# Performance work log

Hardware: AMD Instinct MI355X
Metric: run time of the kernel (lower is better)

Reference implementation:

```python
import jax, jax.numpy as jnp
import numpy as np

B, L, D, H, I = 4, 2048, 768, 12, 3072
HD = D // H  # 64
EPS = 1e-5


def _ln(x, g, b):
    mu = jnp.mean(x, axis=-1, keepdims=True)
    var = jnp.var(x, axis=-1, keepdims=True)
    return (x - mu) * jax.lax.rsqrt(var + EPS) * g + b


def setup_inputs() -> dict:
    key = jax.random.key(0)
    ks = jax.random.split(key, 8)
    s = 0.02
    return {
        "x": jax.random.normal(ks[0], (B, L, D), dtype=jnp.float32),
        "attention_mask": jnp.ones((B, L), dtype=bool),
        "ln1_g": jnp.ones((D,), jnp.float32),
        "ln1_b": jnp.zeros((D,), jnp.float32),
        "w_qkv": jax.random.normal(ks[1], (D, 3 * D), jnp.float32) * s,
        "b_qkv": jnp.zeros((3 * D,), jnp.float32),
        "w_o": jax.random.normal(ks[2], (D, D), jnp.float32) * s,
        "b_o": jnp.zeros((D,), jnp.float32),
        "ln2_g": jnp.ones((D,), jnp.float32),
        "ln2_b": jnp.zeros((D,), jnp.float32),
        "w1": jax.random.normal(ks[3], (D, I), jnp.float32) * s,
        "b1": jnp.zeros((I,), jnp.float32),
        "w2": jax.random.normal(ks[4], (I, D), jnp.float32) * s,
        "b2": jnp.zeros((D,), jnp.float32),
    }


def reference(x, attention_mask, ln1_g, ln1_b, w_qkv, b_qkv, w_o, b_o,
              ln2_g, ln2_b, w1, b1, w2, b2):
    # pre-LN + fused qkv projection
    h = _ln(x, ln1_g, ln1_b)
    qkv = h @ w_qkv + b_qkv                      # [B,L,3D]
    qkv = qkv.reshape(B, L, H, 3 * HD)           # chunk per-head: first HD=q, then k, then v
    q, k, v = qkv[..., :HD], qkv[..., HD:2 * HD], qkv[..., 2 * HD:]
    # NOTE: original divides by head_dim (q.size(-1)), NOT sqrt(head_dim)
    scores = jnp.einsum('blhd,bmhd->bhlm', q, k) / HD   # [B,H,L,L]
    causal = jnp.tril(jnp.ones((L, L), dtype=bool))
    full_mask = attention_mask[:, None, None, :] & causal
    scores = jnp.where(full_mask, scores, -jnp.inf)
    p = jax.nn.softmax(scores, axis=-1)
    attn = jnp.einsum('bhlm,bmhd->blhd', p, v).reshape(B, L, D)
    out_attn = attn @ w_o + b_o + x
    # FFN: Sequential(Linear, Linear, GELU, Dropout) -> GELU applied LAST (faithful to source)
    h2 = _ln(out_attn, ln2_g, ln2_b)
    ff = jax.nn.gelu((h2 @ w1 + b1) @ w2 + b2, approximate=False)
    return out_attn + ff
```

## Files before the change

### kernel.cpp

```cpp
#include <hip/hip_runtime.h>
#include <stdint.h>

typedef __attribute__((ext_vector_type(8))) short short8;
typedef __attribute__((ext_vector_type(4))) float f32x4;

typedef const void __attribute__((address_space(1)))* gas1_t;
typedef void __attribute__((address_space(3)))* las3_t;
#define GLL16(g, l) __builtin_amdgcn_global_load_lds((gas1_t)(const void*)(g), (las3_t)(void*)(l), 16, 0, 0)

__device__ __forceinline__ unsigned short f2bf(float x){
  union { float f; unsigned u; } c; c.f = x;
  return (unsigned short)((c.u + 0x7fffu + ((c.u >> 16) & 1u)) >> 16);
}

__device__ __forceinline__ short8 pack_bf16x8(f32x4 a, f32x4 b){
  union { unsigned u[4]; short8 s8; } r;
  asm("v_cvt_pk_bf16_f32 %0, %1, %2" : "=v"(r.u[0]) : "v"(a[0]), "v"(a[1]));
  asm("v_cvt_pk_bf16_f32 %0, %1, %2" : "=v"(r.u[1]) : "v"(a[2]), "v"(a[3]));
  asm("v_cvt_pk_bf16_f32 %0, %1, %2" : "=v"(r.u[2]) : "v"(b[0]), "v"(b[1]));
  asm("v_cvt_pk_bf16_f32 %0, %1, %2" : "=v"(r.u[3]) : "v"(b[2]), "v"(b[3]));
  return r.s8;
}

constexpr int Bc = 4, Lc = 2048, Dc = 768, Hc = 12, HDc = 64, Ic = 3072;
constexpr int Mrows = Bc * Lc;
constexpr int N3 = 3 * Dc;

__global__ void transpose_w(const float* __restrict__ W, unsigned short* __restrict__ Wt, int K, int N){
  __shared__ float t[32][33];
  int n0 = blockIdx.x * 32, k0 = blockIdx.y * 32;
  int tx = threadIdx.x, ty = threadIdx.y;
  #pragma unroll
  for (int j = 0; j < 4; ++j)
    t[ty + 8*j][tx] = W[(size_t)(k0 + ty + 8*j) * N + n0 + tx];
  __syncthreads();
  #pragma unroll
  for (int j = 0; j < 4; ++j)
    Wt[(size_t)(n0 + ty + 8*j) * K + k0 + tx] = f2bf(t[tx][ty + 8*j]);
}

__global__ void transpose_v(const unsigned short* __restrict__ qkv, unsigned short* __restrict__ vt){
  __shared__ unsigned short t[32][33];
  int l0 = blockIdx.x * 32, d0 = blockIdx.y * 32;
  int bh = blockIdx.z; int b = bh / Hc, h = bh - b * Hc;
  int tx = threadIdx.x, ty = threadIdx.y;
  const unsigned short* src = qkv + (size_t)b * Lc * N3 + h * 192 + 128;
  #pragma unroll
  for (int j = 0; j < 4; ++j)
    t[ty + 8*j][tx] = src[(size_t)(l0 + ty + 8*j) * N3 + d0 + tx];
  __syncthreads();
  unsigned short* dst = vt + (size_t)bh * 64 * Lc;
  #pragma unroll
  for (int j = 0; j < 4; ++j)
    dst[(size_t)(d0 + ty + 8*j) * Lc + l0 + tx] = t[tx][ty + 8*j];
}

__global__ __launch_bounds__(256) void ln_kernel(const float* __restrict__ x, const float* __restrict__ g,
                                                 const float* __restrict__ bta, unsigned short* __restrict__ out){
  int row = blockIdx.x, tid = threadIdx.x;
  const float* xr = x + (size_t)row * 768;
  float v0 = xr[tid], v1 = xr[tid + 256], v2 = xr[tid + 512];
  float s = v0 + v1 + v2;
  float ss = v0*v0 + v1*v1 + v2*v2;
  #pragma unroll
  for (int o = 32; o > 0; o >>= 1){ s += __shfl_xor(s, o); ss += __shfl_xor(ss, o); }
  __shared__ float red[8];
  int w = tid >> 6;
  if ((tid & 63) == 0){ red[w] = s; red[4 + w] = ss; }
  __syncthreads();
  s  = red[0] + red[1] + red[2] + red[3];
  ss = red[4] + red[5] + red[6] + red[7];
  float mu  = s * (1.f / 768.f);
  float var = ss * (1.f / 768.f) - mu * mu;
  float rs  = rsqrtf(var + 1e-5f);
  unsigned short* orow = out + (size_t)row * 768;
  orow[tid]       = f2bf((v0 - mu) * rs * g[tid]       + bta[tid]);
  orow[tid + 256] = f2bf((v1 - mu) * rs * g[tid + 256] + bta[tid + 256]);
  orow[tid + 512] = f2bf((v2 - mu) * rs * g[tid + 512] + bta[tid + 512]);
}

template<int MODE>
__global__ __launch_bounds__(256, 2) void gemm_bt(
    const unsigned short* __restrict__ A, const unsigned short* __restrict__ Bt,
    const float* __restrict__ bias, const float* __restrict__ res,
    void* __restrict__ outp, int Kdim, int Ndim)
{
  __shared__ __align__(16) unsigned short Als[2][128 * 64];
  __shared__ __align__(16) unsigned short Bls[2][128 * 64];
  int tid = threadIdx.x, w = tid >> 6, lane = tid & 63;
  int g = lane >> 4, r16 = lane & 15;

  int nwg = gridDim.x * gridDim.y;
  int flat = blockIdx.y * gridDim.x + blockIdx.x;
  int cpx = nwg >> 3;
  int swz = (flat & 7) * cpx + (flat >> 3);
  int bx = swz % gridDim.x, by = swz / gridDim.x;
  int m0 = by * 128, n0 = bx * 128;
  int wr = (w >> 1) * 64, wc = (w & 1) * 64;

  f32x4 acc[4][4];
  #pragma unroll
  for (int m = 0; m < 4; ++m)
    #pragma unroll
    for (int n = 0; n < 4; ++n) acc[m][n] = f32x4{0.f, 0.f, 0.f, 0.f};

  int lrow = lane >> 3;
  int gsw8 = ((lane & 7) ^ lrow) * 8;
  auto stage = [&](int buf, int kt){
    int k0 = kt * 64;
    #pragma unroll
    for (int i = 0; i < 4; ++i){
      int c = w * 4 + i;
      int row = c * 8 + lrow;
      GLL16(A  + (size_t)(m0 + row) * Kdim + k0 + gsw8, &Als[buf][c * 512]);
      GLL16(Bt + (size_t)(n0 + row) * Kdim + k0 + gsw8, &Bls[buf][c * 512]);
    }
  };

  int nk = Kdim >> 6;
  stage(0, 0);
  int cur = 0;
  for (int kt = 0; kt < nk; ++kt){
    __builtin_amdgcn_s_barrier();
    if (kt + 1 < nk){
      stage(cur ^ 1, kt + 1);
      asm volatile("s_waitcnt vmcnt(8)" ::: "memory");
    } else {
      asm volatile("s_waitcnt vmcnt(0)" ::: "memory");
    }
    __builtin_amdgcn_s_barrier();

    #pragma unroll
    for (int ks = 0; ks < 2; ++ks){
      short8 af[4], bfv[4];
      #pragma unroll
      for (int m = 0; m < 4; ++m){
        int r = wr + m*16 + r16;
        af[m] = *(const short8*)&Als[cur][r * 64 + (((ks*4 + g) ^ (r & 7)) << 3)];
      }
      #pragma unroll
      for (int n = 0; n < 4; ++n){
        int r = wc + n*16 + r16;
        bfv[n] = *(const short8*)&Bls[cur][r * 64 + (((ks*4 + g) ^ (r & 7)) << 3)];
      }
      #pragma unroll
      for (int m = 0; m < 4; ++m)
        #pragma unroll
        for (int n = 0; n < 4; ++n)
          acc[m][n] = __builtin_amdgcn_mfma_f32_16x16x32_bf16(af[m], bfv[n], acc[m][n], 0, 0, 0);
    }
    cur ^= 1;
  }

  #pragma unroll
  for (int n = 0; n < 4; ++n){
    int col = n0 + wc + n*16 + r16;
    float bv = bias[col];
    #pragma unroll
    for (int m = 0; m < 4; ++m){
      #pragma unroll
      for (int j = 0; j < 4; ++j){
        int rowg = m0 + wr + m*16 + g*4 + j;
        size_t idx = (size_t)rowg * Ndim + col;
        float v = acc[m][n][j] + bv;
        if (MODE == 0){
          ((unsigned short*)outp)[idx] = f2bf(v);
        } else if (MODE == 1){
          ((float*)outp)[idx] = v + res[idx];
        } else {
          float ge = 0.5f * v * (1.0f + erff(v * 0.70710678118f));
          ((float*)outp)[idx] = res[idx] + ge;
        }
      }
    }
  }
}

__global__ __launch_bounds__(256, 2) void attn_kernel(const unsigned short* __restrict__ qkv,
                                                      const unsigned short* __restrict__ vt,
                                                      unsigned short* __restrict__ attn_out){
  int qt = 31 - blockIdx.y;
  int bh = blockIdx.x;
  int b = bh / Hc, h = bh - b * Hc;
  int tid = threadIdx.x, w = tid >> 6, lane = tid & 63;
  int g = lane >> 4, r16 = lane & 15;
  const unsigned short* base  = qkv + (size_t)b * Lc * N3 + h * 192;
  const unsigned short* vbase = vt + (size_t)bh * 64 * Lc;

  __shared__ __align__(16) unsigned short Kls[2][64 * 64];
  __shared__ __align__(16) unsigned short Vls[2][64 * 64];
  __shared__ __align__(16) float Pls[4][16 * 64];

  int qw = qt * 64 + w * 16;
  short8 qf[2];
  #pragma unroll
  for (int dh = 0; dh < 2; ++dh)
    qf[dh] = *(const short8*)(base + (size_t)(qw + r16) * N3 + dh*32 + g*8);

  f32x4 o[4];
  #pragma unroll
  for (int nd = 0; nd < 4; ++nd) o[nd] = f32x4{0.f, 0.f, 0.f, 0.f};
  float l_part[4] = {0.f, 0.f, 0.f, 0.f};

  float* Pw = &Pls[w][0];
  constexpr float SM_SCALE = 0.022542110013890052f;

  int lrow = lane >> 3, csw8 = ((lane & 7) ^ lrow) * 8;
  auto stage = [&](int buf, int kt){
    #pragma unroll
    for (int i = 0; i < 2; ++i){
      int r0 = (w * 2 + i) * 8;
      int row = r0 + lrow;
      GLL16(base  + (size_t)(kt*64 + row) * N3 + 64 + csw8, &Kls[buf][r0 * 64]);
      GLL16(vbase + (size_t)row * Lc + kt*64 + csw8,        &Vls[buf][r0 * 64]);
    }
  };

  auto compute_tile = [&](int cur, int kt, bool diag){
    f32x4 s[4];
    #pragma unroll
    for (int nk = 0; nk < 4; ++nk) s[nk] = f32x4{0.f,0.f,0.f,0.f};
    #pragma unroll
    for (int nk = 0; nk < 4; ++nk){
      int krow = nk*16 + r16;
      #pragma unroll
      for (int dh = 0; dh < 2; ++dh){
        short8 kf = *(const short8*)&Kls[cur][krow * 64 + (((dh*4 + g) ^ (krow & 7)) << 3)];
        s[nk] = __builtin_amdgcn_mfma_f32_16x16x32_bf16(qf[dh], kf, s[nk], 0, 0, 0);
      }
    }
    int qv = qw + g*4;
    #pragma unroll
    for (int nk = 0; nk < 4; ++nk){
      int kc = kt*64 + nk*16 + r16;
      #pragma unroll
      for (int j = 0; j < 4; ++j){
        float t = s[nk][j] * SM_SCALE;
        if (diag) t = (kc <= qv + j) ? t : -1e30f;
        float p = __builtin_amdgcn_exp2f(t);
        l_part[j] += p;
        int row = g*4 + j, col = nk*16 + r16;
        Pw[(row << 6) + ((((col >> 2) ^ (row & 7)) << 2) | (col & 3))] = p;
      }
    }
    asm volatile("" ::: "memory");
    #pragma unroll
    for (int ks = 0; ks < 2; ++ks){
      int gr0 = (ks*8 + g*2) ^ (r16 & 7);
      int gr1 = (ks*8 + g*2 + 1) ^ (r16 & 7);
      f32x4 pa = *(const f32x4*)&Pw[(r16 << 6) + (gr0 << 2)];
      f32x4 pb = *(const f32x4*)&Pw[(r16 << 6) + (gr1 << 2)];
      short8 pf = pack_bf16x8(pa, pb);
      #pragma unroll
      for (int nd = 0; nd < 4; ++nd){
        int vrow = nd*16 + r16;
        short8 vf = *(const short8*)&Vls[cur][vrow * 64 + (((ks*4 + g) ^ (vrow & 7)) << 3)];
        o[nd] = __builtin_amdgcn_mfma_f32_16x16x32_bf16(pf, vf, o[nd], 0, 0, 0);
      }
    }
  };

  stage(0, 0);
  __syncthreads();
  int cur = 0;
  for (int kt = 0; kt < qt; ++kt){
    stage(cur ^ 1, kt + 1);
    compute_tile(cur, kt, false);
    __syncthreads();
    cur ^= 1;
  }
  compute_tile(cur, qt, true);

  #pragma unroll
  for (int off = 8; off > 0; off >>= 1)
    #pragma unroll
    for (int j = 0; j < 4; ++j) l_part[j] += __shfl_xor(l_part[j], off);
  float inv[4];
  #pragma unroll
  for (int j = 0; j < 4; ++j) inv[j] = 1.0f / l_part[j];

  unsigned short* ob = attn_out + (size_t)b * Lc * Dc + h * HDc;
  #pragma unroll
  for (int nd = 0; nd < 4; ++nd)
    #pragma unroll
    for (int j = 0; j < 4; ++j){
      int q2 = qw + g*4 + j;
      ob[(size_t)q2 * Dc + nd*16 + r16] = f2bf(o[nd][j] * inv[j]);
    }
}

extern "C" void kernel_launch(void* const* d_in, const int* in_sizes, int n_in,
                              void* d_out, int out_size, void* d_ws, size_t ws_size,
                              hipStream_t stream){
  const float* x     = (const float*)d_in[0];
  const float* ln1_g = (const float*)d_in[2];
  const float* ln1_b = (const float*)d_in[3];
  const float* w_qkv = (const float*)d_in[4];
  const float* b_qkv = (const float*)d_in[5];
  const float* w_o   = (const float*)d_in[6];
  const float* b_o   = (const float*)d_in[7];
  const float* ln2_g = (const float*)d_in[8];
  const float* ln2_b = (const float*)d_in[9];
  const float* w1    = (const float*)d_in[10];
  const float* b1    = (const float*)d_in[11];
  const float* w2    = (const float*)d_in[12];
  const float* b2    = (const float*)d_in[13];

  char* ws = (char*)d_ws;
  size_t off = 0;
  auto alloc = [&](size_t bytes){ void* p = ws + off; off += (bytes + 255) & ~(size_t)255; return p; };
  unsigned short* wqkv_t = (unsigned short*)alloc((size_t)N3 * Dc * 2);
  unsigned short* wo_t   = (unsigned short*)alloc((size_t)Dc * Dc * 2);
  unsigned short* w1_t   = (unsigned short*)alloc((size_t)Ic * Dc * 2);
  unsigned short* w2_t   = (unsigned short*)alloc((size_t)Dc * Ic * 2);
  unsigned short* hbuf   = (unsigned short*)alloc((size_t)Mrows * Dc * 2);
  float*          oattn  = (float*)alloc((size_t)Mrows * Dc * 4);
  unsigned short* vtb    = (unsigned short*)alloc((size_t)Bc * Hc * HDc * Lc * 2);
  char*           big    = (char*)alloc((size_t)Mrows * Ic * 2);
  unsigned short* qkv    = (unsigned short*)big;
  unsigned short* attn_o = (unsigned short*)(big + (size_t)Mrows * N3 * 2);
  unsigned short* ff1    = (unsigned short*)big;

  dim3 tb(32, 8, 1);
  transpose_w<<<dim3(N3/32, Dc/32), tb, 0, stream>>>(w_qkv, wqkv_t, Dc, N3);
  transpose_w<<<dim3(Dc/32, Dc/32), tb, 0, stream>>>(w_o,   wo_t,   Dc, Dc);
  transpose_w<<<dim3(Ic/32, Dc/32), tb, 0, stream>>>(w1,    w1_t,   Dc, Ic);
  transpose_w<<<dim3(Dc/32, Ic/32), tb, 0, stream>>>(w2,    w2_t,   Ic, Dc);

  ln_kernel<<<dim3(Mrows), dim3(256), 0, stream>>>(x, ln1_g, ln1_b, hbuf);

  gemm_bt<0><<<dim3(N3/128, Mrows/128), dim3(256), 0, stream>>>(hbuf, wqkv_t, b_qkv, nullptr, (void*)qkv, Dc, N3);

  transpose_v<<<dim3(Lc/32, HDc/32, Bc*Hc), tb, 0, stream>>>(qkv, vtb);

  attn_kernel<<<dim3(Bc*Hc, Lc/64), dim3(256), 0, stream>>>(qkv, vtb, attn_o);

  gemm_bt<1><<<dim3(Dc/128, Mrows/128), dim3(256), 0, stream>>>(attn_o, wo_t, b_o, x, (void*)oattn, Dc, Dc);

  ln_kernel<<<dim3(Mrows), dim3(256), 0, stream>>>(oattn, ln2_g, ln2_b, hbuf);

  gemm_bt<0><<<dim3(Ic/128, Mrows/128), dim3(256), 0, stream>>>(hbuf, w1_t, b1, nullptr, (void*)ff1, Dc, Ic);

  gemm_bt<2><<<dim3(Dc/128, Mrows/128), dim3(256), 0, stream>>>(ff1, w2_t, b2, oattn, d_out, Ic, Dc);
}
```

Before: 280.8 us.

## Replace 128x128 GEMM with 256x256 eight-wave kernel and interleaved LDS/MFMA phases

All four GEMMs move from a 128x128 tile with 4 waves to a 256x256 tile with 8 waves, each wave computing 128x64. The inner k-loop is split into four phases that alternate LDS fragment loads with MFMA bursts, separated by barriers and s_setprio, so that fragment reads overlap with matrix math and register pressure stays bounded. The larger tiles cut global and LDS traffic per FLOP. In exchange, LDS use reaches 128KB per block and the N=768 GEMMs launch only 96 workgroups, which may leave many CUs idle.

```diff
diff --git a/kernel.cpp b/kernel.cpp
--- a/kernel.cpp
+++ b/kernel.cpp
@@ -80,27 +80,27 @@
 }
 
 template<int MODE>
-__global__ __launch_bounds__(256, 2) void gemm_bt(
+__global__ __launch_bounds__(512, 2) void gemm256(
     const unsigned short* __restrict__ A, const unsigned short* __restrict__ Bt,
     const float* __restrict__ bias, const float* __restrict__ res,
     void* __restrict__ outp, int Kdim, int Ndim)
 {
-  __shared__ __align__(16) unsigned short Als[2][128 * 64];
-  __shared__ __align__(16) unsigned short Bls[2][128 * 64];
+  __shared__ __align__(16) unsigned short Als[2][256 * 64];
+  __shared__ __align__(16) unsigned short Bls[2][256 * 64];
   int tid = threadIdx.x, w = tid >> 6, lane = tid & 63;
   int g = lane >> 4, r16 = lane & 15;
+  int wm = w >> 2, wn = w & 3;
 
   int nwg = gridDim.x * gridDim.y;
   int flat = blockIdx.y * gridDim.x + blockIdx.x;
   int cpx = nwg >> 3;
   int swz = (flat & 7) * cpx + (flat >> 3);
   int bx = swz % gridDim.x, by = swz / gridDim.x;
-  int m0 = by * 128, n0 = bx * 128;
-  int wr = (w >> 1) * 64, wc = (w & 1) * 64;
-
-  f32x4 acc[4][4];
-  #pragma unroll
-  for (int m = 0; m < 4; ++m)
+  int m0 = by * 256, n0 = bx * 256;
+
+  f32x4 acc[8][4];
+  #pragma unroll
+  for (int m = 0; m < 8; ++m)
     #pragma unroll
     for (int n = 0; n < 4; ++n) acc[m][n] = f32x4{0.f, 0.f, 0.f, 0.f};
 
@@ -117,12 +117,23 @@
     }
   };
 
-  int nk = Kdim >> 6;
+  int NK = Kdim >> 6;
+  int cur = 0;
+  auto ldA = [&](int m, int ks) -> short8 {
+    int r = wm * 128 + m * 16 + r16;
+    return *(const short8*)&Als[cur][r * 64 + (((ks*4 + g) ^ (r & 7)) << 3)];
+  };
+  auto ldB = [&](int n, int ks) -> short8 {
+    int r = wn * 64 + n * 16 + r16;
+    return *(const short8*)&Bls[cur][r * 64 + (((ks*4 + g) ^ (r & 7)) << 3)];
+  };
+
   stage(0, 0);
-  int cur = 0;
-  for (int kt = 0; kt < nk; ++kt){
-    __builtin_amdgcn_s_barrier();
-    if (kt + 1 < nk){
+  asm volatile("s_waitcnt vmcnt(0)" ::: "memory");
+  __builtin_amdgcn_s_barrier();
+
+  for (int kt = 0; kt < NK; ++kt){
+    if (kt + 1 < NK){
       stage(cur ^ 1, kt + 1);
       asm volatile("s_waitcnt vmcnt(8)" ::: "memory");
     } else {
@@ -130,37 +141,68 @@
     }
     __builtin_amdgcn_s_barrier();
 
-    #pragma unroll
-    for (int ks = 0; ks < 2; ++ks){
-      short8 af[4], bfv[4];
-      #pragma unroll
-      for (int m = 0; m < 4; ++m){
-        int r = wr + m*16 + r16;
-        af[m] = *(const short8*)&Als[cur][r * 64 + (((ks*4 + g) ^ (r & 7)) << 3)];
-      }
-      #pragma unroll
-      for (int n = 0; n < 4; ++n){
-        int r = wc + n*16 + r16;
-        bfv[n] = *(const short8*)&Bls[cur][r * 64 + (((ks*4 + g) ^ (r & 7)) << 3)];
-      }
-      #pragma unroll
-      for (int m = 0; m < 4; ++m)
+    short8 afr[4][2], bfr[4][2];
+    #pragma unroll
+    for (int m = 0; m < 4; ++m){ afr[m][0] = ldA(m, 0); afr[m][1] = ldA(m, 1); }
+    #pragma unroll
+    for (int n = 0; n < 2; ++n){ bfr[n][0] = ldB(n, 0); bfr[n][1] = ldB(n, 1); }
+    __builtin_amdgcn_s_barrier();
+    __builtin_amdgcn_s_setprio(1);
+    #pragma unroll
+    for (int m = 0; m < 4; ++m)
+      #pragma unroll
+      for (int n = 0; n < 2; ++n)
         #pragma unroll
-        for (int n = 0; n < 4; ++n)
-          acc[m][n] = __builtin_amdgcn_mfma_f32_16x16x32_bf16(af[m], bfv[n], acc[m][n], 0, 0, 0);
-    }
+        for (int ks = 0; ks < 2; ++ks)
+          acc[m][n] = __builtin_amdgcn_mfma_f32_16x16x32_bf16(afr[m][ks], bfr[n][ks], acc[m][n], 0, 0, 0);
+    __builtin_amdgcn_s_setprio(0);
+    #pragma unroll
+    for (int n = 2; n < 4; ++n){ bfr[n][0] = ldB(n, 0); bfr[n][1] = ldB(n, 1); }
+    __builtin_amdgcn_s_barrier();
+    __builtin_amdgcn_s_setprio(1);
+    #pragma unroll
+    for (int m = 0; m < 4; ++m)
+      #pragma unroll
+      for (int n = 2; n < 4; ++n)
+        #pragma unroll
+        for (int ks = 0; ks < 2; ++ks)
+          acc[m][n] = __builtin_amdgcn_mfma_f32_16x16x32_bf16(afr[m][ks], bfr[n][ks], acc[m][n], 0, 0, 0);
+    __builtin_amdgcn_s_setprio(0);
+    #pragma unroll
+    for (int m = 0; m < 4; ++m){ afr[m][0] = ldA(m + 4, 0); afr[m][1] = ldA(m + 4, 1); }
+    __builtin_amdgcn_s_barrier();
+    __builtin_amdgcn_s_setprio(1);
+    #pragma unroll
+    for (int m = 0; m < 4; ++m)
+      #pragma unroll
+      for (int n = 2; n < 4; ++n)
+        #pragma unroll
+        for (int ks = 0; ks < 2; ++ks)
+          acc[m + 4][n] = __builtin_amdgcn_mfma_f32_16x16x32_bf16(afr[m][ks], bfr[n][ks], acc[m + 4][n], 0, 0, 0);
+    __builtin_amdgcn_s_setprio(0);
+    __builtin_amdgcn_s_barrier();
+    __builtin_amdgcn_s_setprio(1);
+    #pragma unroll
+    for (int m = 0; m < 4; ++m)
+      #pragma unroll
+      for (int n = 0; n < 2; ++n)
+        #pragma unroll
+        for (int ks = 0; ks < 2; ++ks)
+          acc[m + 4][n] = __builtin_amdgcn_mfma_f32_16x16x32_bf16(afr[m][ks], bfr[n][ks], acc[m + 4][n], 0, 0, 0);
+    __builtin_amdgcn_s_setprio(0);
+    asm volatile("" ::: "memory");
     cur ^= 1;
   }
 
   #pragma unroll
   for (int n = 0; n < 4; ++n){
-    int col = n0 + wc + n*16 + r16;
+    int col = n0 + wn * 64 + n * 16 + r16;
     float bv = bias[col];
     #pragma unroll
-    for (int m = 0; m < 4; ++m){
+    for (int m = 0; m < 8; ++m){
       #pragma unroll
       for (int j = 0; j < 4; ++j){
-        int rowg = m0 + wr + m*16 + g*4 + j;
+        int rowg = m0 + wm * 128 + m * 16 + g * 4 + j;
         size_t idx = (size_t)rowg * Ndim + col;
         float v = acc[m][n][j] + bv;
         if (MODE == 0){
@@ -329,17 +371,17 @@
 
   ln_kernel<<<dim3(Mrows), dim3(256), 0, stream>>>(x, ln1_g, ln1_b, hbuf);
 
-  gemm_bt<0><<<dim3(N3/128, Mrows/128), dim3(256), 0, stream>>>(hbuf, wqkv_t, b_qkv, nullptr, (void*)qkv, Dc, N3);
+  gemm256<0><<<dim3(N3/256, Mrows/256), dim3(512), 0, stream>>>(hbuf, wqkv_t, b_qkv, nullptr, (void*)qkv, Dc, N3);
 
   transpose_v<<<dim3(Lc/32, HDc/32, Bc*Hc), tb, 0, stream>>>(qkv, vtb);
 
   attn_kernel<<<dim3(Bc*Hc, Lc/64), dim3(256), 0, stream>>>(qkv, vtb, attn_o);
 
-  gemm_bt<1><<<dim3(Dc/128, Mrows/128), dim3(256), 0, stream>>>(attn_o, wo_t, b_o, x, (void*)oattn, Dc, Dc);
+  gemm256<1><<<dim3(Dc/256, Mrows/256), dim3(512), 0, stream>>>(attn_o, wo_t, b_o, x, (void*)oattn, Dc, Dc);
 
   ln_kernel<<<dim3(Mrows), dim3(256), 0, stream>>>(oattn, ln2_g, ln2_b, hbuf);
 
-  gemm_bt<0><<<dim3(Ic/128, Mrows/128), dim3(256), 0, stream>>>(hbuf, w1_t, b1, nullptr, (void*)ff1, Dc, Ic);
-
-  gemm_bt<2><<<dim3(Dc/128, Mrows/128), dim3(256), 0, stream>>>(ff1, w2_t, b2, oattn, d_out, Ic, Dc);
-}
+  gemm256<0><<<dim3(Ic/256, Mrows/256), dim3(512), 0, stream>>>(hbuf, w1_t, b1, nullptr, (void*)ff1, Dc, Ic);
+
+  gemm256<2><<<dim3(Dc/256, Mrows/256), dim3(512), 0, stream>>>(ff1, w2_t, b2, oattn, d_out, Ic, Dc);
+}
```

Result: slower. 384.6 us (+36.9%).

## Add 256x256 eight-wave ping-pong GEMM for QKV and FFN1 projections

Applied to the files above, without the earlier changes.

Adds a new GEMM kernel with 512 threads and a 256x256 output tile, used for the QKV and first FFN projections. Each wave owns a 128x64 output sub-tile. LDS loads of fragments, asynchronous global-to-LDS staging of the next K tiles and MFMA quarter-blocks are interleaved with barriers and s_setprio to overlap memory and compute. The larger tile raises data reuse per byte loaded but uses 128KB of LDS, limiting each CU to one block, and yields fewer blocks (288 and 384) to spread across the CUs, which risks tail imbalance. The older 128-tile GEMM also reorders its staging loads into two halves.

```diff
diff --git a/kernel.cpp b/kernel.cpp
--- a/kernel.cpp
+++ b/kernel.cpp
@@ -79,6 +79,147 @@
   orow[tid + 512] = f2bf((v2 - mu) * rs * g[tid + 512] + bta[tid + 512]);
 }
 
+__global__ __launch_bounds__(512, 2) void gemm256(
+    const unsigned short* __restrict__ A, const unsigned short* __restrict__ Bt,
+    const float* __restrict__ bias, unsigned short* __restrict__ outp,
+    int Kdim, int Ndim)
+{
+  __shared__ __align__(16) unsigned short Als[2][256 * 64];
+  __shared__ __align__(16) unsigned short Bls[2][256 * 64];
+  int tid = threadIdx.x, w = tid >> 6, lane = tid & 63;
+  int g = lane >> 4, r16 = lane & 15;
+  int wm = w >> 2, wn = w & 3;
+
+  int nwg = gridDim.x * gridDim.y;
+  int flat = blockIdx.y * gridDim.x + blockIdx.x;
+  int cpx = nwg >> 3;
+  int swz = (flat & 7) * cpx + (flat >> 3);
+  int bx = swz % gridDim.x, by = swz / gridDim.x;
+  int m0 = by * 256, n0 = bx * 256;
+
+  f32x4 acc[8][4];
+  #pragma unroll
+  for (int m = 0; m < 8; ++m)
+    #pragma unroll
+    for (int n = 0; n < 4; ++n) acc[m][n] = f32x4{0.f, 0.f, 0.f, 0.f};
+
+  int lrow = lane >> 3;
+  int gsw8 = ((lane & 7) ^ lrow) * 8;
+
+  auto stageA = [&](int buf, int kt, int mh){
+    int k0 = kt * 64;
+    #pragma unroll
+    for (int i = 0; i < 2; ++i){
+      int lr0 = w * 16 + i * 8;
+      int r0 = ((lr0 & 64) << 1) | (mh << 6) | (lr0 & 63);
+      GLL16(A + (size_t)(m0 + r0 + lrow) * Kdim + k0 + gsw8, &Als[buf][r0 * 64]);
+    }
+  };
+  auto stageB = [&](int buf, int kt, int nh){
+    int k0 = kt * 64;
+    #pragma unroll
+    for (int i = 0; i < 2; ++i){
+      int lr0 = w * 16 + i * 8;
+      int r0 = ((lr0 & 96) << 1) | (nh << 5) | (lr0 & 31);
+      GLL16(Bt + (size_t)(n0 + r0 + lrow) * Kdim + k0 + gsw8, &Bls[buf][r0 * 64]);
+    }
+  };
+
+  auto ldA = [&](int buf, int m, int ks) -> short8 {
+    int r = wm * 128 + m * 16 + r16;
+    return *(const short8*)&Als[buf][r * 64 + (((ks*4 + g) ^ (r & 7)) << 3)];
+  };
+  auto ldB = [&](int buf, int n, int ks) -> short8 {
+    int r = wn * 64 + n * 16 + r16;
+    return *(const short8*)&Bls[buf][r * 64 + (((ks*4 + g) ^ (r & 7)) << 3)];
+  };
+
+#define LDA4(AF, BUF, MB) { _Pragma("unroll") for (int m_ = 0; m_ < 4; ++m_){ AF[m_][0] = ldA(BUF, MB + m_, 0); AF[m_][1] = ldA(BUF, MB + m_, 1); } }
+#define LDB2(BF, BUF, NB) { _Pragma("unroll") for (int n_ = 0; n_ < 2; ++n_){ BF[n_][0] = ldB(BUF, NB + n_, 0); BF[n_][1] = ldB(BUF, NB + n_, 1); } }
+#define QMFMA(MB, NB, AF, BF) { \
+  __builtin_amdgcn_s_setprio(1); \
+  _Pragma("unroll") for (int m_ = 0; m_ < 4; ++m_) \
+  _Pragma("unroll") for (int n_ = 0; n_ < 2; ++n_) \
+  _Pragma("unroll") for (int k_ = 0; k_ < 2; ++k_) \
+    acc[(MB)+m_][(NB)+n_] = __builtin_amdgcn_mfma_f32_16x16x32_bf16(AF[m_][k_], BF[n_][k_], acc[(MB)+m_][(NB)+n_], 0, 0, 0); \
+  __builtin_amdgcn_s_setprio(0); }
+#define BAR() __builtin_amdgcn_s_barrier()
+
+  int NK = Kdim >> 6;
+  int NITER = NK >> 1;
+
+  stageA(0, 0, 0); stageB(0, 0, 1); stageA(0, 0, 1); stageB(0, 0, 0);
+  stageA(1, 1, 0); stageB(1, 1, 1);
+
+  short8 af0[4][2], af1[4][2], bf0[2][2], bf1[2][2];
+
+  for (int it = 0; it < NITER; ++it){
+    int t = 2 * it;
+    bool lastIt = (it == NITER - 1);
+
+    asm volatile("s_waitcnt vmcnt(4)" ::: "memory");
+    BAR();
+    LDA4(af0, 0, 0); LDB2(bf0, 0, 0);
+    stageA(1, t + 1, 1);
+    QMFMA(0, 0, af0, bf0);
+    BAR();
+    LDB2(bf1, 0, 2);
+    stageB(1, t + 1, 0);
+    BAR();
+    QMFMA(0, 2, af0, bf1);
+    BAR();
+    LDA4(af1, 0, 4);
+    if (t + 2 < NK) stageA(0, t + 2, 0);
+    BAR();
+    QMFMA(4, 2, af1, bf1);
+    BAR();
+    if (t + 2 < NK) stageB(0, t + 2, 1);
+    BAR();
+    QMFMA(4, 0, af1, bf0);
+    BAR();
+    if (lastIt) { asm volatile("s_waitcnt vmcnt(0)" ::: "memory"); }
+    else        { asm volatile("s_waitcnt vmcnt(4)" ::: "memory"); }
+    BAR();
+    LDA4(af0, 1, 0); LDB2(bf0, 1, 0);
+    if (t + 2 < NK) stageA(0, t + 2, 1);
+    QMFMA(0, 0, af0, bf0);
+    BAR();
+    LDB2(bf1, 1, 2);
+    if (t + 2 < NK) stageB(0, t + 2, 0);
+    BAR();
+    QMFMA(0, 2, af0, bf1);
+    BAR();
+    LDA4(af1, 1, 4);
+    if (t + 3 < NK) stageA(1, t + 3, 0);
+    BAR();
+    QMFMA(4, 2, af1, bf1);
+    BAR();
+    if (t + 3 < NK) stageB(1, t + 3, 1);
+    BAR();
+    QMFMA(4, 0, af1, bf0);
+    BAR();
+  }
+
+#undef LDA4
+#undef LDB2
+#undef QMFMA
+#undef BAR
+
+  #pragma unroll
+  for (int n = 0; n < 4; ++n){
+    int col = n0 + wn * 64 + n * 16 + r16;
+    float bv = bias[col];
+    #pragma unroll
+    for (int m = 0; m < 8; ++m){
+      #pragma unroll
+      for (int j = 0; j < 4; ++j){
+        int rowg = m0 + wm * 128 + m * 16 + g * 4 + j;
+        outp[(size_t)rowg * Ndim + col] = f2bf(acc[m][n][j] + bv);
+      }
+    }
+  }
+}
+
 template<int MODE>
 __global__ __launch_bounds__(256, 2) void gemm_bt(
     const unsigned short* __restrict__ A, const unsigned short* __restrict__ Bt,
@@ -109,21 +250,31 @@
   auto stage = [&](int buf, int kt){
     int k0 = kt * 64;
     #pragma unroll
-    for (int i = 0; i < 4; ++i){
-      int c = w * 4 + i;
+    for (int i = 0; i < 2; ++i){
+      int c = w * 2 + i;
       int row = c * 8 + lrow;
       GLL16(A  + (size_t)(m0 + row) * Kdim + k0 + gsw8, &Als[buf][c * 512]);
       GLL16(Bt + (size_t)(n0 + row) * Kdim + k0 + gsw8, &Bls[buf][c * 512]);
     }
   };
+  auto stage2 = [&](int buf, int kt){
+    int k0 = kt * 64;
+    #pragma unroll
+    for (int i = 2; i < 4; ++i){
+      int c = w * 2 + (i - 2) + 8;
+      int row = c * 8 + lrow;
+      GLL16(A  + (size_t)(m0 + row) * Kdim + k0 + gsw8, &Als[buf][c * 512]);
+      GLL16(Bt + (size_t)(n0 + row) * Kdim + k0 + gsw8, &Bls[buf][c * 512]);
+    }
+  };
 
   int nk = Kdim >> 6;
-  stage(0, 0);
+  stage(0, 0); stage2(0, 0);
   int cur = 0;
   for (int kt = 0; kt < nk; ++kt){
     __builtin_amdgcn_s_barrier();
     if (kt + 1 < nk){
-      stage(cur ^ 1, kt + 1);
+      stage(cur ^ 1, kt + 1); stage2(cur ^ 1, kt + 1);
       asm volatile("s_waitcnt vmcnt(8)" ::: "memory");
     } else {
       asm volatile("s_waitcnt vmcnt(0)" ::: "memory");
@@ -329,7 +480,7 @@
 
   ln_kernel<<<dim3(Mrows), dim3(256), 0, stream>>>(x, ln1_g, ln1_b, hbuf);
 
-  gemm_bt<0><<<dim3(N3/128, Mrows/128), dim3(256), 0, stream>>>(hbuf, wqkv_t, b_qkv, nullptr, (void*)qkv, Dc, N3);
+  gemm256<<<dim3(N3/256, Mrows/256), dim3(512), 0, stream>>>(hbuf, wqkv_t, b_qkv, qkv, Dc, N3);
 
   transpose_v<<<dim3(Lc/32, HDc/32, Bc*Hc), tb, 0, stream>>>(qkv, vtb);
 
@@ -339,7 +490,7 @@
 
   ln_kernel<<<dim3(Mrows), dim3(256), 0, stream>>>(oattn, ln2_g, ln2_b, hbuf);
 
-  gemm_bt<0><<<dim3(Ic/128, Mrows/128), dim3(256), 0, stream>>>(hbuf, w1_t, b1, nullptr, (void*)ff1, Dc, Ic);
+  gemm256<<<dim3(Ic/256, Mrows/256), dim3(512), 0, stream>>>(hbuf, w1_t, b1, ff1, Dc, Ic);
 
   gemm_bt<2><<<dim3(Dc/128, Mrows/128), dim3(256), 0, stream>>>(ff1, w2_t, b2, oattn, d_out, Ic, Dc);
 }
```

Result: slower. 298.4 us (+6.2%).
